# Optimization experiments

Measured on AMD Instinct MI355X. Metric: run time of the kernel, lower is better.

## Reference

```python
import jax, jax.numpy as jnp
import numpy as np

NUM_PATCHES = 4
PATCH_RADIUS = 0.2


def setup_inputs() -> dict:
    key = jax.random.key(0)
    points = jax.random.normal(key, (64, 65536, 6), dtype=jnp.float32)
    return {"points": points}


def _fps(xyz, n_samples):
    """Furthest point sampling (pointnet2 convention: start at index 0).
    xyz: (B, N, 3) -> (B, n_samples) int32 indices."""
    B, N, _ = xyz.shape

    def body(carry, _):
        min_d, last_idx = carry                                   # (B,N), (B,)
        last = jnp.take_along_axis(xyz, last_idx[:, None, None], axis=1)  # (B,1,3)
        d = jnp.sum((xyz - last) ** 2, axis=-1)                   # (B,N)
        min_d = jnp.minimum(min_d, d)
        nxt = jnp.argmax(min_d, axis=1).astype(jnp.int32)
        return (min_d, nxt), last_idx

    init = (jnp.full((B, N), 1e10, dtype=xyz.dtype),
            jnp.zeros((B,), dtype=jnp.int32))
    (_, _), idxs = jax.lax.scan(body, init, None, length=n_samples)
    return idxs.T                                                  # (B, n_samples)


def reference(points):
    B, N, C = points.shape
    xyz = points[..., :3]

    # 1) pick patch centers via FPS
    centers_idx = _fps(xyz, NUM_PATCHES)                           # (B,P)
    centers = jnp.take_along_axis(xyz, centers_idx[..., None], axis=1)  # (B,P,3)

    # 2) distance of every point to nearest center -> drop mask
    dist = jnp.linalg.norm(xyz[:, :, None, :] - centers[:, None, :, :], axis=-1)  # (B,N,P)
    min_dist = jnp.min(dist, axis=2)                               # (B,N)
    keep = min_dist >= PATCH_RADIUS                                # (B,N) bool, True = kept

    # 3) stable compaction: kept points first (original order preserved),
    #    then repeat-fill pattern valid_points[j % num_valid]
    order = jnp.argsort(jnp.logical_not(keep).astype(jnp.int32), axis=1, stable=True)  # (B,N)
    num_valid = jnp.sum(keep, axis=1)                              # (B,)
    j = jnp.arange(N, dtype=jnp.int32)[None, :]                    # (1,N)
    k = j % jnp.maximum(num_valid, 1)[:, None]                     # (B,N)
    src = jnp.take_along_axis(order, k, axis=1)                    # (B,N)
    out = jnp.take_along_axis(points, src[..., None], axis=1)      # (B,N,C)

    # all points dropped -> zeros (matches torch branch)
    return jnp.where((num_valid > 0)[:, None, None], out, jnp.zeros_like(out))
```

## Files before the change

### kernel.cpp

```cpp
#include <hip/hip_runtime.h>
#include <stdint.h>

#define NN 65536
#define BB 64
#define TPB 256

#define BPB 16
#define GRID_BLKS (BB * BPB)
#define PPB 4096
#define LPT 16

#define FBPB 32
#define FGRID (BB * FBPB)
#define FPPB 2048
#define FLPT 8
#define GBPB 16
#define GGRID (BB * GBPB)
#define GLPT 16

__device__ __forceinline__ float sqdist(float x, float y, float z,
                                        float cx, float cy, float cz) {
    float dx = __fsub_rn(x, cx);
    float dy = __fsub_rn(y, cy);
    float dz = __fsub_rn(z, cz);
    return __fadd_rn(__fadd_rn(__fmul_rn(dx, dx), __fmul_rn(dy, dy)),
                     __fmul_rn(dz, dz));
}

__device__ __forceinline__ unsigned long long pack_key(float v, int i) {
    return ((unsigned long long)__float_as_uint(v) << 32) |
           (unsigned long long)(0xFFFFFFFFu - (unsigned)i);
}

__device__ __forceinline__ int key_idx(unsigned long long key) {
    return (int)(0xFFFFFFFFu - (unsigned)(key & 0xFFFFFFFFu));
}

__device__ __forceinline__ void batch_barrier(unsigned* cnt, unsigned* gen) {
    __syncthreads();
    if (threadIdx.x == 0) {
        unsigned g = __hip_atomic_load(gen, __ATOMIC_RELAXED,
                                       __HIP_MEMORY_SCOPE_AGENT);
        unsigned a = __hip_atomic_fetch_add(cnt, 1u, __ATOMIC_ACQ_REL,
                                            __HIP_MEMORY_SCOPE_AGENT) + 1u;
        if (a == (unsigned)BPB) {
            __hip_atomic_store(cnt, 0u, __ATOMIC_RELAXED,
                               __HIP_MEMORY_SCOPE_AGENT);
            __hip_atomic_store(gen, g + 1u, __ATOMIC_RELEASE,
                               __HIP_MEMORY_SCOPE_AGENT);
        } else {
            while (__hip_atomic_load(gen, __ATOMIC_RELAXED,
                                     __HIP_MEMORY_SCOPE_AGENT) == g)
                __builtin_amdgcn_s_sleep(4);
            __builtin_amdgcn_fence(__ATOMIC_ACQUIRE, "agent");
        }
    }
    __syncthreads();
}

__global__ void init_barrier(unsigned* bar) {
    const int t = threadIdx.x;
    bar[t * 32 + 0] = 0u;
    bar[t * 32 + 1] = 0u;
}

__global__ __launch_bounds__(TPB, 4) void fused_kernel(
        const float* __restrict__ pts,
        unsigned long long* __restrict__ partKey,
        uint64_t* __restrict__ masks,
        float* __restrict__ out,
        unsigned* __restrict__ bar) {
    const int gb = blockIdx.x;
    const int b = gb >> 4, blk = gb & 15;
    const int tid = threadIdx.x;
    const int lane = tid & 63, wid = tid >> 6;
    const float* base = pts + (size_t)b * NN * 6;
    unsigned* bcnt = bar + b * 32;
    unsigned* bgen = bar + b * 32 + 1;

    __shared__ unsigned long long s_k[4];
    __shared__ float s_c[3];
    __shared__ uint64_t s_m[1024];
    __shared__ int s_pre[1024];
    __shared__ int s_ws[4], s_wo[4];
    __shared__ int s_nv;

    float px[LPT], py[LPT], pz[LPT], md[LPT];
    #pragma unroll
    for (int l = 0; l < LPT; ++l) {
        const int p = blk * PPB + l * TPB + tid;
        const float* q = base + (size_t)p * 6;
        float2 xy = *(const float2*)q;
        px[l] = xy.x; py[l] = xy.y; pz[l] = q[2];
        asm volatile("" : "+v"(px[l]), "+v"(py[l]), "+v"(pz[l]));
    }

    float cx = base[0], cy = base[1], cz = base[2];
    #pragma unroll
    for (int l = 0; l < LPT; ++l)
        md[l] = sqdist(px[l], py[l], pz[l], cx, cy, cz);

    for (int k = 0; k < 3; ++k) {
        float bestv = -1.0f; int besti = 0x7fffffff;
        #pragma unroll
        for (int l = 0; l < LPT; ++l) {
            if (md[l] > bestv) { bestv = md[l]; besti = blk * PPB + l * TPB + tid; }
        }
        unsigned long long key = pack_key(bestv, besti);
        #pragma unroll
        for (int off = 32; off > 0; off >>= 1) {
            unsigned long long ok = __shfl_down(key, off, 64);
            if (ok > key) key = ok;
        }
        if (lane == 0) s_k[wid] = key;
        __syncthreads();
        if (tid == 0) {
            unsigned long long bk = s_k[0];
            #pragma unroll
            for (int w = 1; w < 4; ++w) bk = (s_k[w] > bk) ? s_k[w] : bk;
            partKey[k * GRID_BLKS + gb] = bk;
        }
        batch_barrier(bcnt, bgen);

        if (tid == 0) {
            const unsigned long long* s = partKey + k * GRID_BLKS + b * BPB;
            unsigned long long bk = s[0];
            #pragma unroll
            for (int w = 1; w < BPB; ++w) bk = (s[w] > bk) ? s[w] : bk;
            const float* cp = base + (size_t)key_idx(bk) * 6;
            s_c[0] = cp[0]; s_c[1] = cp[1]; s_c[2] = cp[2];
        }
        __syncthreads();
        cx = s_c[0]; cy = s_c[1]; cz = s_c[2];
        #pragma unroll
        for (int l = 0; l < LPT; ++l)
            md[l] = fminf(md[l], sqdist(px[l], py[l], pz[l], cx, cy, cz));
    }

    uint64_t* mb = masks + (size_t)b * 1024;
    #pragma unroll
    for (int l = 0; l < LPT; ++l) {
        int keep = (__fsqrt_rn(md[l]) >= 0.2f) ? 1 : 0;
        uint64_t m = __ballot(keep);
        if (lane == 0) mb[blk * 64 + l * 4 + wid] = m;
    }
    batch_barrier(bcnt, bgen);

    uint64_t w[4];
    int cnt = 0;
    #pragma unroll
    for (int kk = 0; kk < 4; ++kk) {
        w[kk] = mb[tid * 4 + kk];
        s_m[tid * 4 + kk] = w[kk];
        cnt += __popcll(w[kk]);
    }
    int incl = cnt;
    #pragma unroll
    for (int off = 1; off < 64; off <<= 1) {
        int v = __shfl_up(incl, off, 64);
        if (lane >= off) incl += v;
    }
    if (lane == 63) s_ws[wid] = incl;
    __syncthreads();
    if (tid == 0) {
        int run = 0;
        #pragma unroll
        for (int q = 0; q < 4; ++q) { s_wo[q] = run; run += s_ws[q]; }
        s_nv = run;
    }
    __syncthreads();
    int run = s_wo[wid] + incl - cnt;
    #pragma unroll
    for (int kk = 0; kk < 4; ++kk) {
        s_pre[tid * 4 + kk] = run;
        run += __popcll(w[kk]);
    }
    __syncthreads();

    const int nv = s_nv;
    float* ob = out + (size_t)b * NN * 6;

    if (nv <= 0) {
        float2 zz = make_float2(0.f, 0.f);
        #pragma unroll
        for (int l = 0; l < LPT; ++l) {
            int j = blk * PPB + l * TPB + tid;
            float2* o = (float2*)(ob + (size_t)j * 6);
            o[0] = zz; o[1] = zz; o[2] = zz;
        }
        return;
    }

    #pragma unroll
    for (int l = 0; l < LPT; ++l) {
        int j = blk * PPB + l * TPB + tid;
        int jj = (int)((unsigned)j % (unsigned)nv);
        int wd = 0;
        #pragma unroll
        for (int s = 512; s > 0; s >>= 1) {
            int cand = wd + s;
            if (cand < 1024 && s_pre[cand] <= jj) wd = cand;
        }
        int r = jj - s_pre[wd];
        uint64_t m = s_m[wd];
        int bit = 0;
        int c = __popcll(m & 0xFFFFFFFFull);
        if (r >= c) { r -= c; m >>= 32; bit += 32; }
        c = __popcll(m & 0xFFFFull);
        if (r >= c) { r -= c; m >>= 16; bit += 16; }
        c = __popcll(m & 0xFFull);
        if (r >= c) { r -= c; m >>= 8; bit += 8; }
        c = __popcll(m & 0xFull);
        if (r >= c) { r -= c; m >>= 4; bit += 4; }
        c = __popcll(m & 0x3ull);
        if (r >= c) { r -= c; m >>= 2; bit += 2; }
        if (r >= (int)(m & 1ull)) { bit += 1; }
        int src = wd * 64 + bit;
        const float2* p = (const float2*)(base + (size_t)src * 6);
        float2* o = (float2*)(ob + (size_t)j * 6);
        float2 r0 = p[0], r1 = p[1], r2 = p[2];
        o[0] = r0; o[1] = r1; o[2] = r2;
    }
}

__device__ __forceinline__ int reduce_part(const unsigned long long* partKey,
                                           int a, int b) {
    const unsigned long long* s = partKey + a * FGRID + b * FBPB;
    unsigned long long bk = s[0];
    #pragma unroll
    for (int w = 1; w < FBPB; ++w) bk = (s[w] > bk) ? s[w] : bk;
    return key_idx(bk);
}

template<int NC>
__global__ __launch_bounds__(TPB) void fps_pass(
        const float* __restrict__ pts, unsigned long long* partKey) {
    const int gb = blockIdx.x;
    const int b = gb >> 5, blk = gb & 31;
    const int tid = threadIdx.x;
    const int lane = tid & 63, wid = tid >> 6;
    const float* base = pts + (size_t)b * NN * 6;

    float cx[NC], cy[NC], cz[NC];
    cx[0] = base[0]; cy[0] = base[1]; cz[0] = base[2];
    #pragma unroll
    for (int k = 1; k < NC; ++k) {
        int idx = reduce_part(partKey, k - 1, b);
        const float* p = base + (size_t)idx * 6;
        cx[k] = p[0]; cy[k] = p[1]; cz[k] = p[2];
    }

    float bestv = -1.0f; int besti = 0x7fffffff;
    #pragma unroll
    for (int l = 0; l < FLPT; ++l) {
        const int p = blk * FPPB + l * TPB + tid;
        const float* q = base + (size_t)p * 6;
        float2 xy = *(const float2*)q;
        float  zz = q[2];
        float d = sqdist(xy.x, xy.y, zz, cx[0], cy[0], cz[0]);
        #pragma unroll
        for (int k = 1; k < NC; ++k)
            d = fminf(d, sqdist(xy.x, xy.y, zz, cx[k], cy[k], cz[k]));
        if (d > bestv) { bestv = d; besti = p; }
    }
    unsigned long long key = pack_key(bestv, besti);
    #pragma unroll
    for (int off = 32; off > 0; off >>= 1) {
        unsigned long long ok = __shfl_down(key, off, 64);
        if (ok > key) key = ok;
    }
    __shared__ unsigned long long s_k[4];
    if (lane == 0) s_k[wid] = key;
    __syncthreads();
    if (tid == 0) {
        unsigned long long bk = s_k[0];
        #pragma unroll
        for (int w = 1; w < 4; ++w) bk = (s_k[w] > bk) ? s_k[w] : bk;
        partKey[(NC - 1) * FGRID + gb] = bk;
    }
}

__global__ __launch_bounds__(TPB) void fps_final(
        const float* __restrict__ pts,
        const unsigned long long* __restrict__ partKey,
        uint64_t* __restrict__ masks) {
    const int gb = blockIdx.x;
    const int b = gb >> 5, blk = gb & 31;
    const int tid = threadIdx.x;
    const int lane = tid & 63, wid = tid >> 6;
    const float* base = pts + (size_t)b * NN * 6;

    float cx[4], cy[4], cz[4];
    cx[0] = base[0]; cy[0] = base[1]; cz[0] = base[2];
    #pragma unroll
    for (int k = 1; k < 4; ++k) {
        int idx = reduce_part(partKey, k - 1, b);
        const float* p = base + (size_t)idx * 6;
        cx[k] = p[0]; cy[k] = p[1]; cz[k] = p[2];
    }
    uint64_t* mb = masks + (size_t)b * 1024;

    #pragma unroll
    for (int l = 0; l < FLPT; ++l) {
        const int p = blk * FPPB + l * TPB + tid;
        const float* q = base + (size_t)p * 6;
        float2 xy = *(const float2*)q;
        float  zz = q[2];
        float d = sqdist(xy.x, xy.y, zz, cx[0], cy[0], cz[0]);
        #pragma unroll
        for (int k = 1; k < 4; ++k)
            d = fminf(d, sqdist(xy.x, xy.y, zz, cx[k], cy[k], cz[k]));
        int keep = (__fsqrt_rn(d) >= 0.2f) ? 1 : 0;
        uint64_t m = __ballot(keep);
        if (lane == 0) mb[blk * 32 + l * 4 + wid] = m;
    }
}

__global__ __launch_bounds__(TPB) void gather_kernel(
        const float* __restrict__ pts, const uint64_t* __restrict__ masks,
        float* __restrict__ out) {
    const int gb = blockIdx.x;
    const int b = gb >> 4, blk = gb & 15;
    const int tid = threadIdx.x;
    const int lane = tid & 63, wid = tid >> 6;
    __shared__ uint64_t s_m[1024];
    __shared__ int s_pre[1024];
    __shared__ int s_ws[4], s_wo[4];
    __shared__ int s_nv;

    const uint64_t* mb = masks + (size_t)b * 1024;
    uint64_t w[4];
    int cnt = 0;
    #pragma unroll
    for (int k = 0; k < 4; ++k) {
        w[k] = mb[tid * 4 + k];
        s_m[tid * 4 + k] = w[k];
        cnt += __popcll(w[k]);
    }
    int incl = cnt;
    #pragma unroll
    for (int off = 1; off < 64; off <<= 1) {
        int v = __shfl_up(incl, off, 64);
        if (lane >= off) incl += v;
    }
    if (lane == 63) s_ws[wid] = incl;
    __syncthreads();
    if (tid == 0) {
        int run = 0;
        #pragma unroll
        for (int q = 0; q < 4; ++q) { s_wo[q] = run; run += s_ws[q]; }
        s_nv = run;
    }
    __syncthreads();
    int run = s_wo[wid] + incl - cnt;
    #pragma unroll
    for (int k = 0; k < 4; ++k) {
        s_pre[tid * 4 + k] = run;
        run += __popcll(w[k]);
    }
    __syncthreads();

    const int nv = s_nv;
    const float* baseP = pts + (size_t)b * NN * 6;
    float* ob = out + (size_t)b * NN * 6;

    if (nv <= 0) {
        float2 zz = make_float2(0.f, 0.f);
        #pragma unroll
        for (int l = 0; l < GLPT; ++l) {
            int j = blk * 4096 + l * TPB + tid;
            float2* o = (float2*)(ob + (size_t)j * 6);
            o[0] = zz; o[1] = zz; o[2] = zz;
        }
        return;
    }

    #pragma unroll
    for (int l = 0; l < GLPT; ++l) {
        int j = blk * 4096 + l * TPB + tid;
        int jj = (int)((unsigned)j % (unsigned)nv);
        int wd = 0;
        #pragma unroll
        for (int s = 512; s > 0; s >>= 1) {
            int cand = wd + s;
            if (cand < 1024 && s_pre[cand] <= jj) wd = cand;
        }
        int r = jj - s_pre[wd];
        uint64_t m = s_m[wd];
        int bit = 0;
        int c = __popcll(m & 0xFFFFFFFFull);
        if (r >= c) { r -= c; m >>= 32; bit += 32; }
        c = __popcll(m & 0xFFFFull);
        if (r >= c) { r -= c; m >>= 16; bit += 16; }
        c = __popcll(m & 0xFFull);
        if (r >= c) { r -= c; m >>= 8; bit += 8; }
        c = __popcll(m & 0xFull);
        if (r >= c) { r -= c; m >>= 4; bit += 4; }
        c = __popcll(m & 0x3ull);
        if (r >= c) { r -= c; m >>= 2; bit += 2; }
        if (r >= (int)(m & 1ull)) { bit += 1; }
        int src = wd * 64 + bit;
        const float2* p = (const float2*)(baseP + (size_t)src * 6);
        float2* o = (float2*)(ob + (size_t)j * 6);
        float2 r0 = p[0], r1 = p[1], r2 = p[2];
        o[0] = r0; o[1] = r1; o[2] = r2;
    }
}

extern "C" void kernel_launch(void* const* d_in, const int* in_sizes, int n_in,
                              void* d_out, int out_size, void* d_ws, size_t ws_size,
                              hipStream_t stream) {
    const float* pts = (const float*)d_in[0];
    float* out = (float*)d_out;

    unsigned long long* partKey = (unsigned long long*)d_ws;
    unsigned* bar = (unsigned*)((char*)d_ws + (48 << 10));
    uint64_t* masks = (uint64_t*)((char*)d_ws + (64 << 10));

    static int fused_ok = -1;
    if (fused_ok < 0) {
        int dev = 0;
        (void)hipGetDevice(&dev);
        int ncu = 0, nb = 0;
        hipError_t e1 = hipDeviceGetAttribute(&ncu, hipDeviceAttributeMultiprocessorCount, dev);
        hipError_t e2 = hipOccupancyMaxActiveBlocksPerMultiprocessor(
            &nb, (const void*)fused_kernel, TPB, 0);
        fused_ok = (e1 == hipSuccess && e2 == hipSuccess &&
                    (long)nb * (long)ncu >= (long)GRID_BLKS) ? 1 : 0;
    }

    if (fused_ok) {
        init_barrier<<<1, 64, 0, stream>>>(bar);
        fused_kernel<<<GRID_BLKS, TPB, 0, stream>>>(pts, partKey, masks, out, bar);
    } else {
        fps_pass<1><<<FGRID, TPB, 0, stream>>>(pts, partKey);
        fps_pass<2><<<FGRID, TPB, 0, stream>>>(pts, partKey);
        fps_pass<3><<<FGRID, TPB, 0, stream>>>(pts, partKey);
        fps_final<<<FGRID, TPB, 0, stream>>>(pts, partKey, masks);
        gather_kernel<<<GGRID, TPB, 0, stream>>>(pts, masks, out);
    }
}
```

Before: 244.9 us.

## Scatter kept points by rank, fill tail separately, and use 32 blocks per batch

The fused kernel is templated on blocks per batch and points per thread, and a 32-block, 8-point-per-thread configuration is preferred when occupancy allows all blocks to be co-resident. Compaction now writes each kept point directly to its rank, computed from ballot masks and prefix sums. Only the repeat-filled tail uses the binary search plus select-bit lookup. The cross-block argmax is done with a wave shuffle in every wave instead of a single thread and shared memory. This trades more grid-barrier participants and scattered writes for less per-output search work and more parallelism.

```diff
diff --git a/kernel.cpp b/kernel.cpp
--- a/kernel.cpp
+++ b/kernel.cpp
@@ -4,11 +4,6 @@
 #define NN 65536
 #define BB 64
 #define TPB 256
-
-#define BPB 16
-#define GRID_BLKS (BB * BPB)
-#define PPB 4096
-#define LPT 16
 
 #define FBPB 32
 #define FGRID (BB * FBPB)
@@ -31,11 +26,27 @@
     return ((unsigned long long)__float_as_uint(v) << 32) |
            (unsigned long long)(0xFFFFFFFFu - (unsigned)i);
 }
-
 __device__ __forceinline__ int key_idx(unsigned long long key) {
     return (int)(0xFFFFFFFFu - (unsigned)(key & 0xFFFFFFFFu));
 }
 
+__device__ __forceinline__ int sel_bit(uint64_t m, int r) {
+    int bit = 0;
+    int c = __popcll(m & 0xFFFFFFFFull);
+    if (r >= c) { r -= c; m >>= 32; bit += 32; }
+    c = __popcll(m & 0xFFFFull);
+    if (r >= c) { r -= c; m >>= 16; bit += 16; }
+    c = __popcll(m & 0xFFull);
+    if (r >= c) { r -= c; m >>= 8; bit += 8; }
+    c = __popcll(m & 0xFull);
+    if (r >= c) { r -= c; m >>= 4; bit += 4; }
+    c = __popcll(m & 0x3ull);
+    if (r >= c) { r -= c; m >>= 2; bit += 2; }
+    if (r >= (int)(m & 1ull)) { bit += 1; }
+    return bit;
+}
+
+template<int NB>
 __device__ __forceinline__ void batch_barrier(unsigned* cnt, unsigned* gen) {
     __syncthreads();
     if (threadIdx.x == 0) {
@@ -43,7 +54,7 @@
                                        __HIP_MEMORY_SCOPE_AGENT);
         unsigned a = __hip_atomic_fetch_add(cnt, 1u, __ATOMIC_ACQ_REL,
                                             __HIP_MEMORY_SCOPE_AGENT) + 1u;
-        if (a == (unsigned)BPB) {
+        if (a == (unsigned)NB) {
             __hip_atomic_store(cnt, 0u, __ATOMIC_RELAXED,
                                __HIP_MEMORY_SCOPE_AGENT);
             __hip_atomic_store(gen, g + 1u, __ATOMIC_RELEASE,
@@ -64,14 +75,18 @@
     bar[t * 32 + 1] = 0u;
 }
 
-__global__ __launch_bounds__(TPB, 4) void fused_kernel(
+template<int BPBT, int LPTT, int MINW>
+__global__ __launch_bounds__(TPB, MINW) void fused_kernel(
         const float* __restrict__ pts,
         unsigned long long* __restrict__ partKey,
         uint64_t* __restrict__ masks,
         float* __restrict__ out,
         unsigned* __restrict__ bar) {
+    constexpr int PPBT = NN / BPBT;
+    constexpr int WPB  = PPBT / 64;
+    constexpr int GRIDT = BB * BPBT;
     const int gb = blockIdx.x;
-    const int b = gb >> 4, blk = gb & 15;
+    const int b = gb / BPBT, blk = gb % BPBT;
     const int tid = threadIdx.x;
     const int lane = tid & 63, wid = tid >> 6;
     const float* base = pts + (size_t)b * NN * 6;
@@ -79,16 +94,15 @@
     unsigned* bgen = bar + b * 32 + 1;
 
     __shared__ unsigned long long s_k[4];
-    __shared__ float s_c[3];
     __shared__ uint64_t s_m[1024];
     __shared__ int s_pre[1024];
     __shared__ int s_ws[4], s_wo[4];
     __shared__ int s_nv;
 
-    float px[LPT], py[LPT], pz[LPT], md[LPT];
-    #pragma unroll
-    for (int l = 0; l < LPT; ++l) {
-        const int p = blk * PPB + l * TPB + tid;
+    float px[LPTT], py[LPTT], pz[LPTT], md[LPTT];
+    #pragma unroll
+    for (int l = 0; l < LPTT; ++l) {
+        const int p = blk * PPBT + l * TPB + tid;
         const float* q = base + (size_t)p * 6;
         float2 xy = *(const float2*)q;
         px[l] = xy.x; py[l] = xy.y; pz[l] = q[2];
@@ -97,14 +111,14 @@
 
     float cx = base[0], cy = base[1], cz = base[2];
     #pragma unroll
-    for (int l = 0; l < LPT; ++l)
+    for (int l = 0; l < LPTT; ++l)
         md[l] = sqdist(px[l], py[l], pz[l], cx, cy, cz);
 
     for (int k = 0; k < 3; ++k) {
         float bestv = -1.0f; int besti = 0x7fffffff;
         #pragma unroll
-        for (int l = 0; l < LPT; ++l) {
-            if (md[l] > bestv) { bestv = md[l]; besti = blk * PPB + l * TPB + tid; }
+        for (int l = 0; l < LPTT; ++l) {
+            if (md[l] > bestv) { bestv = md[l]; besti = blk * PPBT + l * TPB + tid; }
         }
         unsigned long long key = pack_key(bestv, besti);
         #pragma unroll
@@ -118,33 +132,32 @@
             unsigned long long bk = s_k[0];
             #pragma unroll
             for (int w = 1; w < 4; ++w) bk = (s_k[w] > bk) ? s_k[w] : bk;
-            partKey[k * GRID_BLKS + gb] = bk;
-        }
-        batch_barrier(bcnt, bgen);
-
-        if (tid == 0) {
-            const unsigned long long* s = partKey + k * GRID_BLKS + b * BPB;
-            unsigned long long bk = s[0];
-            #pragma unroll
-            for (int w = 1; w < BPB; ++w) bk = (s[w] > bk) ? s[w] : bk;
-            const float* cp = base + (size_t)key_idx(bk) * 6;
-            s_c[0] = cp[0]; s_c[1] = cp[1]; s_c[2] = cp[2];
-        }
-        __syncthreads();
-        cx = s_c[0]; cy = s_c[1]; cz = s_c[2];
-        #pragma unroll
-        for (int l = 0; l < LPT; ++l)
+            partKey[k * GRIDT + gb] = bk;
+        }
+        batch_barrier<BPBT>(bcnt, bgen);
+
+        const unsigned long long* s = partKey + k * GRIDT + b * BPBT;
+        unsigned long long bk = s[lane & (BPBT - 1)];
+        #pragma unroll
+        for (int off = 32; off > 0; off >>= 1) {
+            unsigned long long ok = __shfl_xor(bk, off, 64);
+            if (ok > bk) bk = ok;
+        }
+        const float* cp = base + (size_t)key_idx(bk) * 6;
+        cx = cp[0]; cy = cp[1]; cz = cp[2];
+        #pragma unroll
+        for (int l = 0; l < LPTT; ++l)
             md[l] = fminf(md[l], sqdist(px[l], py[l], pz[l], cx, cy, cz));
     }
 
     uint64_t* mb = masks + (size_t)b * 1024;
     #pragma unroll
-    for (int l = 0; l < LPT; ++l) {
+    for (int l = 0; l < LPTT; ++l) {
         int keep = (__fsqrt_rn(md[l]) >= 0.2f) ? 1 : 0;
         uint64_t m = __ballot(keep);
-        if (lane == 0) mb[blk * 64 + l * 4 + wid] = m;
-    }
-    batch_barrier(bcnt, bgen);
+        if (lane == 0) mb[blk * WPB + l * 4 + wid] = m;
+    }
+    batch_barrier<BPBT>(bcnt, bgen);
 
     uint64_t w[4];
     int cnt = 0;
@@ -183,8 +196,8 @@
     if (nv <= 0) {
         float2 zz = make_float2(0.f, 0.f);
         #pragma unroll
-        for (int l = 0; l < LPT; ++l) {
-            int j = blk * PPB + l * TPB + tid;
+        for (int l = 0; l < LPTT; ++l) {
+            int j = blk * PPBT + l * TPB + tid;
             float2* o = (float2*)(ob + (size_t)j * 6);
             o[0] = zz; o[1] = zz; o[2] = zz;
         }
@@ -192,34 +205,38 @@
     }
 
     #pragma unroll
-    for (int l = 0; l < LPT; ++l) {
-        int j = blk * PPB + l * TPB + tid;
-        int jj = (int)((unsigned)j % (unsigned)nv);
-        int wd = 0;
-        #pragma unroll
-        for (int s = 512; s > 0; s >>= 1) {
-            int cand = wd + s;
-            if (cand < 1024 && s_pre[cand] <= jj) wd = cand;
-        }
-        int r = jj - s_pre[wd];
-        uint64_t m = s_m[wd];
-        int bit = 0;
-        int c = __popcll(m & 0xFFFFFFFFull);
-        if (r >= c) { r -= c; m >>= 32; bit += 32; }
-        c = __popcll(m & 0xFFFFull);
-        if (r >= c) { r -= c; m >>= 16; bit += 16; }
-        c = __popcll(m & 0xFFull);
-        if (r >= c) { r -= c; m >>= 8; bit += 8; }
-        c = __popcll(m & 0xFull);
-        if (r >= c) { r -= c; m >>= 4; bit += 4; }
-        c = __popcll(m & 0x3ull);
-        if (r >= c) { r -= c; m >>= 2; bit += 2; }
-        if (r >= (int)(m & 1ull)) { bit += 1; }
-        int src = wd * 64 + bit;
-        const float2* p = (const float2*)(base + (size_t)src * 6);
-        float2* o = (float2*)(ob + (size_t)j * 6);
-        float2 r0 = p[0], r1 = p[1], r2 = p[2];
-        o[0] = r0; o[1] = r1; o[2] = r2;
+    for (int l = 0; l < LPTT; ++l) {
+        const int p = blk * PPBT + l * TPB + tid;
+        const int w_idx = blk * WPB + l * 4 + wid;
+        uint64_t m = s_m[w_idx];
+        int rank = s_pre[w_idx] + __popcll(m & ((1ull << lane) - 1ull));
+        if ((m >> lane) & 1ull) {
+            const float2* q = (const float2*)(base + (size_t)p * 6);
+            float2* o = (float2*)(ob + (size_t)rank * 6);
+            float2 r0 = q[0], r1 = q[1], r2 = q[2];
+            o[0] = r0; o[1] = r1; o[2] = r2;
+        }
+    }
+
+    const int T = NN - nv;
+    if (T > 0) {
+        const int chunk = (T + BPBT - 1) / BPBT;
+        const int j0 = nv + blk * chunk;
+        const int j1 = (j0 + chunk < NN) ? (j0 + chunk) : NN;
+        for (int j = j0 + tid; j < j1; j += TPB) {
+            unsigned jj = (unsigned)j % (unsigned)nv;
+            int wd = 0;
+            #pragma unroll
+            for (int s2 = 512; s2 > 0; s2 >>= 1) {
+                int cand = wd + s2;
+                if (cand < 1024 && s_pre[cand] <= (int)jj) wd = cand;
+            }
+            int src = wd * 64 + sel_bit(s_m[wd], (int)jj - s_pre[wd]);
+            const float2* q = (const float2*)(base + (size_t)src * 6);
+            float2* o = (float2*)(ob + (size_t)j * 6);
+            float2 r0 = q[0], r1 = q[1], r2 = q[2];
+            o[0] = r0; o[1] = r1; o[2] = r2;
+        }
     }
 }
 
@@ -385,21 +402,7 @@
             int cand = wd + s;
             if (cand < 1024 && s_pre[cand] <= jj) wd = cand;
         }
-        int r = jj - s_pre[wd];
-        uint64_t m = s_m[wd];
-        int bit = 0;
-        int c = __popcll(m & 0xFFFFFFFFull);
-        if (r >= c) { r -= c; m >>= 32; bit += 32; }
-        c = __popcll(m & 0xFFFFull);
-        if (r >= c) { r -= c; m >>= 16; bit += 16; }
-        c = __popcll(m & 0xFFull);
-        if (r >= c) { r -= c; m >>= 8; bit += 8; }
-        c = __popcll(m & 0xFull);
-        if (r >= c) { r -= c; m >>= 4; bit += 4; }
-        c = __popcll(m & 0x3ull);
-        if (r >= c) { r -= c; m >>= 2; bit += 2; }
-        if (r >= (int)(m & 1ull)) { bit += 1; }
-        int src = wd * 64 + bit;
+        int src = wd * 64 + sel_bit(s_m[wd], jj - s_pre[wd]);
         const float2* p = (const float2*)(baseP + (size_t)src * 6);
         float2* o = (float2*)(ob + (size_t)j * 6);
         float2 r0 = p[0], r1 = p[1], r2 = p[2];
@@ -417,21 +420,32 @@
     unsigned* bar = (unsigned*)((char*)d_ws + (48 << 10));
     uint64_t* masks = (uint64_t*)((char*)d_ws + (64 << 10));
 
-    static int fused_ok = -1;
-    if (fused_ok < 0) {
+    static int mode = -1;
+    if (mode < 0) {
         int dev = 0;
         (void)hipGetDevice(&dev);
         int ncu = 0, nb = 0;
         hipError_t e1 = hipDeviceGetAttribute(&ncu, hipDeviceAttributeMultiprocessorCount, dev);
         hipError_t e2 = hipOccupancyMaxActiveBlocksPerMultiprocessor(
-            &nb, (const void*)fused_kernel, TPB, 0);
-        fused_ok = (e1 == hipSuccess && e2 == hipSuccess &&
-                    (long)nb * (long)ncu >= (long)GRID_BLKS) ? 1 : 0;
-    }
-
-    if (fused_ok) {
+            &nb, (const void*)fused_kernel<32, 8, 8>, TPB, 0);
+        if (e1 == hipSuccess && e2 == hipSuccess &&
+            (long)nb * (long)ncu >= (long)(BB * 32)) {
+            mode = 2;
+        } else {
+            int nb2 = 0;
+            hipError_t e3 = hipOccupancyMaxActiveBlocksPerMultiprocessor(
+                &nb2, (const void*)fused_kernel<16, 16, 4>, TPB, 0);
+            mode = (e1 == hipSuccess && e3 == hipSuccess &&
+                    (long)nb2 * (long)ncu >= (long)(BB * 16)) ? 1 : 0;
+        }
+    }
+
+    if (mode == 2) {
         init_barrier<<<1, 64, 0, stream>>>(bar);
-        fused_kernel<<<GRID_BLKS, TPB, 0, stream>>>(pts, partKey, masks, out, bar);
+        fused_kernel<32, 8, 8><<<BB * 32, TPB, 0, stream>>>(pts, partKey, masks, out, bar);
+    } else if (mode == 1) {
+        init_barrier<<<1, 64, 0, stream>>>(bar);
+        fused_kernel<16, 16, 4><<<BB * 16, TPB, 0, stream>>>(pts, partKey, masks, out, bar);
     } else {
         fps_pass<1><<<FGRID, TPB, 0, stream>>>(pts, partKey);
         fps_pass<2><<<FGRID, TPB, 0, stream>>>(pts, partKey);
```

Result: no change. 245.8 us (+0.4%).
